# Kernel optimization log

Measured on AMD Instinct MI355X. Metric: run time of the kernel, lower is better.

Reference implementation:

```python
import jax, jax.numpy as jnp
import numpy as np

N = 8192
F_IN = 128
D = 128
NEG_SLOPE = 0.2  # cfg.negativeslope (standard GAT value)
MASK_FILL = -9e15


def setup_inputs() -> dict:
    key = jax.random.key(0)
    k1, k2, k3, k4 = jax.random.split(key, 4)
    A = jax.random.randint(k1, (N, N), 0, 2, dtype=jnp.int32)
    X = jax.random.normal(k2, (N, F_IN), dtype=jnp.float32)
    # glorot init for Ws, xavier_uniform(gain=1.414) for a
    lim_w = float(np.sqrt(6.0 / (F_IN + D)))
    Ws = jax.random.uniform(k3, (F_IN, D), minval=-lim_w, maxval=lim_w, dtype=jnp.float32)
    lim_a = 1.414 * float(np.sqrt(6.0 / (2 * D + 1)))
    a = jax.random.uniform(k4, (2 * D, 1), minval=-lim_a, maxval=lim_a, dtype=jnp.float32)
    return {"A": A, "X": X, "Ws": Ws, "a": a}


def reference(A, X, Ws, a):
    # Wh: [N, D]
    Wh = X @ Ws
    d = Wh.shape[-1]
    # additive attention: e_ij = leaky_relu(Wh_i . a1 + Wh_j . a2)
    e1 = Wh @ a[:d]          # [N, 1]
    e2 = Wh @ a[d:]          # [N, 1]
    e = jax.nn.leaky_relu(e1 + e2.T, negative_slope=NEG_SLOPE)  # [N, N]
    e = jnp.where(A > 0, e, MASK_FILL)
    attn = jax.nn.softmax(e, axis=1)  # row-wise over neighbors
    H = attn @ Wh            # [N, D]
    return H
```

## Files before the change

kernel.cpp:

```cpp
#include <hip/hip_runtime.h>
#include <hip/hip_bf16.h>

#define NN 8192
#define DD 128

typedef __attribute__((ext_vector_type(8))) short short8;
typedef __attribute__((ext_vector_type(4))) float f32x4;
typedef unsigned int u32;

__device__ __forceinline__ ushort f2bf(float f) {
    __hip_bfloat16 h = __float2bfloat16(f);
    return *(ushort*)&h;
}

__device__ __forceinline__ void async_ld16(const void* g, void* l) {
    __builtin_amdgcn_global_load_lds(
        (const __attribute__((address_space(1))) u32*)g,
        (__attribute__((address_space(3))) u32*)l, 16, 0, 0);
}

__global__ __launch_bounds__(128) void k1_gemm(const float* __restrict__ X,
                                               const float* __restrict__ Ws,
                                               float* __restrict__ Wh) {
    __shared__ float lWs[128 * 128];
    __shared__ float lX[32 * 129];
    int t = threadIdx.x, bx = blockIdx.x;
    const float4* Ws4 = (const float4*)Ws;
    float4* lWs4 = (float4*)lWs;
#pragma unroll
    for (int j = 0; j < 32; ++j) lWs4[t + j * 128] = Ws4[t + j * 128];
#pragma unroll
    for (int j = 0; j < 32; ++j) {
        int u = t + j * 128;
        int r = u >> 7, c = u & 127;
        lX[r * 129 + c] = X[(bx * 32 + r) * 128 + c];
    }
    __syncthreads();
    int tr = t >> 4, c = t & 15;
    int r0 = tr * 4;
    float acc[4][8];
#pragma unroll
    for (int i = 0; i < 4; ++i)
#pragma unroll
        for (int j = 0; j < 8; ++j) acc[i][j] = 0.f;
#pragma unroll 4
    for (int k = 0; k < 128; ++k) {
        float x0 = lX[(r0 + 0) * 129 + k];
        float x1 = lX[(r0 + 1) * 129 + k];
        float x2 = lX[(r0 + 2) * 129 + k];
        float x3 = lX[(r0 + 3) * 129 + k];
        float4 w0 = *(const float4*)&lWs[k * 128 + c * 8];
        float4 w1 = *(const float4*)&lWs[k * 128 + c * 8 + 4];
        float wv[8];
        *(float4*)(wv) = w0; *(float4*)(wv + 4) = w1;
#pragma unroll
        for (int j = 0; j < 8; ++j) {
            acc[0][j] += x0 * wv[j];
            acc[1][j] += x1 * wv[j];
            acc[2][j] += x2 * wv[j];
            acc[3][j] += x3 * wv[j];
        }
    }
#pragma unroll
    for (int i = 0; i < 4; ++i) {
        float4* o = (float4*)&Wh[(size_t)(bx * 32 + r0 + i) * 128 + c * 8];
        o[0] = (float4){acc[i][0], acc[i][1], acc[i][2], acc[i][3]};
        o[1] = (float4){acc[i][4], acc[i][5], acc[i][6], acc[i][7]};
    }
}

__global__ void k2_prep(const float* __restrict__ Wh, const float* __restrict__ a,
                        ushort* __restrict__ WhT, float* __restrict__ C1,
                        float* __restrict__ C1s, float* __restrict__ E2p,
                        float* __restrict__ E2n) {
    int wave = threadIdx.x >> 6, lane = threadIdx.x & 63;
    int i = blockIdx.x * 4 + wave;
    int d = lane * 2;
    float wh0 = Wh[i * 128 + d], wh1 = Wh[i * 128 + d + 1];
    float s1 = wh0 * a[d]       + wh1 * a[d + 1];
    float s2 = wh0 * a[128 + d] + wh1 * a[128 + d + 1];
    for (int off = 32; off; off >>= 1) {
        s1 += __shfl_xor(s1, off);
        s2 += __shfl_xor(s2, off);
    }
    WhT[(size_t)d * NN + i]       = f2bf(wh0);
    WhT[(size_t)(d + 1) * NN + i] = f2bf(wh1);
    if (lane == 0) {
        C1[i]  = __expf(s1);
        C1s[i] = __expf(0.2f * s1);
        E2p[i] = __expf(s2);
        E2n[i] = __expf(0.2f * s2);
    }
}

__global__ __launch_bounds__(1024, 8) void k3_main(
    const int* __restrict__ A, const ushort* __restrict__ WhT,
    const float* __restrict__ C1, const float* __restrict__ C1s,
    const float* __restrict__ E2p, const float* __restrict__ E2n,
    float* __restrict__ Hp, float* __restrict__ Lp) {

    __shared__ __align__(16) char tile[2][8192];
    __shared__ float red[4][16][128];
    __shared__ float lsq[2][64];

    int tid = threadIdx.x;
    int lane = tid & 63;
    int wv = tid >> 6;
    int g = wv & 3;
    int s = (wv >> 2) & 1;
    int h = wv >> 3;
    int n = lane & 15;
    int kg = lane >> 4;

    int bx = blockIdx.x;
    int kb = blockIdx.y;
    int row = bx * 64 + g * 16 + n;
    int kbase = kb * 2048 + s * 1024;

    float c1 = C1[row], c1s = C1s[row];
    const int* Arow = A + (size_t)row * NN + kbase + kg * 8;
    const float* Ep = E2p + kbase + kg * 8;
    const float* En = E2n + kbase + kg * 8;
    const ushort* src0 = WhT + (size_t)(h * 64 + g * 16 + n) * NN + kbase + kg * 8;
    char* dst0 = &tile[s][(h * 4 + g) * 1024 + lane * 16];

    f32x4 acc[4];
#pragma unroll
    for (int cc = 0; cc < 4; ++cc) acc[cc] = (f32x4){0.f, 0.f, 0.f, 0.f};
    float lsum = 0.f;

    for (int t = 0; t < 32; ++t) {
        int k = t * 32;
        async_ld16(src0 + k, dst0);
        int4 a0 = *(const int4*)(Arow + k);
        int4 a1 = *(const int4*)(Arow + k + 4);
        float4 pa = *(const float4*)(Ep + k);
        float4 pb = *(const float4*)(Ep + k + 4);
        float4 na = *(const float4*)(En + k);
        float4 nb = *(const float4*)(En + k + 4);
        __syncthreads();
        int am[8]; float ep[8], en[8];
        *(int4*)(am) = a0;       *(int4*)(am + 4) = a1;
        *(float4*)(ep) = pa;     *(float4*)(ep + 4) = pb;
        *(float4*)(en) = na;     *(float4*)(en + 4) = nb;
        short8 af;
#pragma unroll
        for (int u = 0; u < 8; ++u) {
            float w = fmaxf(c1 * ep[u], c1s * en[u]);
            w = am[u] ? w : 0.f;
            lsum += w;
            af[u] = (short)f2bf(w);
        }
#pragma unroll
        for (int cc = 0; cc < 4; ++cc) {
            short8 bf = *(const short8*)&tile[s][(h * 4 + cc) * 1024 + lane * 16];
            acc[cc] = __builtin_amdgcn_mfma_f32_16x16x32_bf16(af, bf, acc[cc], 0, 0, 0);
        }
        __syncthreads();
    }

    lsum += __shfl_xor(lsum, 16);
    lsum += __shfl_xor(lsum, 32);

    if (s == 0) {
#pragma unroll
        for (int cc = 0; cc < 4; ++cc)
#pragma unroll
            for (int r = 0; r < 4; ++r)
                red[g][kg * 4 + r][h * 64 + cc * 16 + n] = acc[cc][r];
        if (h == 0 && lane < 16) lsq[0][g * 16 + lane] = lsum;
    }
    __syncthreads();
    if (s == 1) {
#pragma unroll
        for (int cc = 0; cc < 4; ++cc)
#pragma unroll
            for (int r = 0; r < 4; ++r)
                red[g][kg * 4 + r][h * 64 + cc * 16 + n] += acc[cc][r];
        if (h == 0 && lane < 16) lsq[1][g * 16 + lane] = lsum;
    }
    __syncthreads();

    float* Hpb = Hp + (size_t)kb * (NN * DD) + (size_t)bx * 64 * 128;
    const float* redf = &red[0][0][0];
#pragma unroll
    for (int u = 0; u < 8; ++u) Hpb[tid + u * 1024] = redf[tid + u * 1024];
    if (tid < 64) Lp[kb * NN + bx * 64 + tid] = lsq[0][tid] + lsq[1][tid];
}

__global__ void k4_final(const float* __restrict__ Hp, const float* __restrict__ Lp,
                         float* __restrict__ out) {
    int idx = blockIdx.x * 256 + threadIdx.x;
    int i = idx >> 7;
    float sv = Hp[idx] + Hp[1048576 + idx] + Hp[2097152 + idx] + Hp[3145728 + idx];
    float l = Lp[i] + Lp[8192 + i] + Lp[16384 + i] + Lp[24576 + i];
    out[idx] = sv / l;
}

extern "C" void kernel_launch(void* const* d_in, const int* in_sizes, int n_in,
                              void* d_out, int out_size, void* d_ws, size_t ws_size,
                              hipStream_t stream) {
    const int*   A  = (const int*)d_in[0];
    const float* X  = (const float*)d_in[1];
    const float* Ws = (const float*)d_in[2];
    const float* a  = (const float*)d_in[3];
    float* out = (float*)d_out;

    char* ws = (char*)d_ws;
    float*  Wh  = (float*)(ws);
    ushort* WhT = (ushort*)(ws + (4u << 20));
    float*  C1  = (float*)(ws + (6u << 20));
    float*  C1s = (float*)(ws + (6u << 20) + (32u << 10));
    float*  E2p = (float*)(ws + (6u << 20) + (96u << 10));
    float*  E2n = (float*)(ws + (6u << 20) + (128u << 10));
    float*  Hp  = (float*)(ws + (8u << 20));
    float*  Lp  = (float*)(ws + (24u << 20));

    k1_gemm<<<256, 128, 0, stream>>>(X, Ws, Wh);
    k2_prep<<<2048, 256, 0, stream>>>(Wh, a, WhT, C1, C1s, E2p, E2n);
    k3_main<<<dim3(128, 4), 1024, 0, stream>>>(A, WhT, C1, C1s, E2p, E2n, Hp, Lp);
    k4_final<<<4096, 256, 0, stream>>>(Hp, Lp, out);
}
```

Measured before the change: 473.9 us.

## Stage adjacency and WhT tiles via async LDS double buffering, restructure prep kernels

The main kernel now streams both the adjacency tiles and the bf16 WhT tiles into double-buffered LDS with async global-to-LDS loads. Each wave covers the full 2048-wide K range for 16 rows and 32 output columns, which removes the split-K LDS reduction. Row sums come from an MFMA against a ones vector instead of scalar adds. The GEMM and prep kernels are also rewritten: coalesced float4 loads, an LDS transpose for the bf16 WhT stores, and wider blocks. The trade-off is 128KB of LDS per block and fewer MFMA column tiles per wave, which limits occupancy.

```diff
diff --git a/kernel.cpp b/kernel.cpp
--- a/kernel.cpp
+++ b/kernel.cpp
@@ -19,173 +19,207 @@
         (__attribute__((address_space(3))) u32*)l, 16, 0, 0);
 }
 
-__global__ __launch_bounds__(128) void k1_gemm(const float* __restrict__ X,
+__global__ __launch_bounds__(256) void k1_gemm(const float* __restrict__ X,
                                                const float* __restrict__ Ws,
                                                float* __restrict__ Wh) {
-    __shared__ float lWs[128 * 128];
-    __shared__ float lX[32 * 129];
+    __shared__ float lWs[128 * 132];
+    __shared__ float lX[32 * 132];
     int t = threadIdx.x, bx = blockIdx.x;
     const float4* Ws4 = (const float4*)Ws;
-    float4* lWs4 = (float4*)lWs;
-#pragma unroll
-    for (int j = 0; j < 32; ++j) lWs4[t + j * 128] = Ws4[t + j * 128];
-#pragma unroll
-    for (int j = 0; j < 32; ++j) {
-        int u = t + j * 128;
-        int r = u >> 7, c = u & 127;
-        lX[r * 129 + c] = X[(bx * 32 + r) * 128 + c];
+    const float4* X4 = (const float4*)X;
+    for (int j = 0; j < 16; ++j) {
+        int u = j * 256 + t;
+        int k = u >> 5, c4 = u & 31;
+        *(float4*)&lWs[k * 132 + c4 * 4] = Ws4[u];
+    }
+    for (int j = 0; j < 4; ++j) {
+        int u = j * 256 + t;
+        int r = u >> 5, c4 = u & 31;
+        *(float4*)&lX[r * 132 + c4 * 4] = X4[bx * 1024 + u];
     }
     __syncthreads();
-    int tr = t >> 4, c = t & 15;
-    int r0 = tr * 4;
-    float acc[4][8];
+    int r0 = (t >> 5) * 4, c0 = (t & 31) * 4;
+    float acc[4][4];
 #pragma unroll
     for (int i = 0; i < 4; ++i)
 #pragma unroll
-        for (int j = 0; j < 8; ++j) acc[i][j] = 0.f;
+        for (int j = 0; j < 4; ++j) acc[i][j] = 0.f;
 #pragma unroll 4
     for (int k = 0; k < 128; ++k) {
-        float x0 = lX[(r0 + 0) * 129 + k];
-        float x1 = lX[(r0 + 1) * 129 + k];
-        float x2 = lX[(r0 + 2) * 129 + k];
-        float x3 = lX[(r0 + 3) * 129 + k];
-        float4 w0 = *(const float4*)&lWs[k * 128 + c * 8];
-        float4 w1 = *(const float4*)&lWs[k * 128 + c * 8 + 4];
-        float wv[8];
-        *(float4*)(wv) = w0; *(float4*)(wv + 4) = w1;
-#pragma unroll
-        for (int j = 0; j < 8; ++j) {
-            acc[0][j] += x0 * wv[j];
-            acc[1][j] += x1 * wv[j];
-            acc[2][j] += x2 * wv[j];
-            acc[3][j] += x3 * wv[j];
+        float4 wv = *(const float4*)&lWs[k * 132 + c0];
+        float x0 = lX[(r0 + 0) * 132 + k];
+        float x1 = lX[(r0 + 1) * 132 + k];
+        float x2 = lX[(r0 + 2) * 132 + k];
+        float x3 = lX[(r0 + 3) * 132 + k];
+#pragma unroll
+        for (int j = 0; j < 4; ++j) {
+            acc[0][j] += x0 * ((const float*)&wv)[j];
+            acc[1][j] += x1 * ((const float*)&wv)[j];
+            acc[2][j] += x2 * ((const float*)&wv)[j];
+            acc[3][j] += x3 * ((const float*)&wv)[j];
         }
     }
 #pragma unroll
-    for (int i = 0; i < 4; ++i) {
-        float4* o = (float4*)&Wh[(size_t)(bx * 32 + r0 + i) * 128 + c * 8];
-        o[0] = (float4){acc[i][0], acc[i][1], acc[i][2], acc[i][3]};
-        o[1] = (float4){acc[i][4], acc[i][5], acc[i][6], acc[i][7]};
-    }
-}
-
-__global__ void k2_prep(const float* __restrict__ Wh, const float* __restrict__ a,
-                        ushort* __restrict__ WhT, float* __restrict__ C1,
-                        float* __restrict__ C1s, float* __restrict__ E2p,
-                        float* __restrict__ E2n) {
-    int wave = threadIdx.x >> 6, lane = threadIdx.x & 63;
-    int i = blockIdx.x * 4 + wave;
-    int d = lane * 2;
-    float wh0 = Wh[i * 128 + d], wh1 = Wh[i * 128 + d + 1];
-    float s1 = wh0 * a[d]       + wh1 * a[d + 1];
-    float s2 = wh0 * a[128 + d] + wh1 * a[128 + d + 1];
-    for (int off = 32; off; off >>= 1) {
-        s1 += __shfl_xor(s1, off);
-        s2 += __shfl_xor(s2, off);
-    }
-    WhT[(size_t)d * NN + i]       = f2bf(wh0);
-    WhT[(size_t)(d + 1) * NN + i] = f2bf(wh1);
-    if (lane == 0) {
+    for (int i = 0; i < 4; ++i)
+        *(float4*)&Wh[(size_t)(bx * 32 + r0 + i) * 128 + c0] =
+            (float4){acc[i][0], acc[i][1], acc[i][2], acc[i][3]};
+}
+
+__global__ __launch_bounds__(256) void k2_prep(const float* __restrict__ Wh,
+                                               const float* __restrict__ a,
+                                               ushort* __restrict__ WhT,
+                                               float* __restrict__ C1,
+                                               float* __restrict__ C1s,
+                                               float* __restrict__ E2p,
+                                               float* __restrict__ E2n) {
+    __shared__ float lT[128 * 65];
+    __shared__ float la[256];
+    int t = threadIdx.x;
+    int i0 = blockIdx.x * 64;
+    la[t] = a[t];
+    for (int j = 0; j < 32; ++j) {
+        int u = j * 256 + t;
+        int r = u >> 7, c = u & 127;
+        lT[c * 65 + r] = Wh[(size_t)(i0 + r) * 128 + c];
+    }
+    __syncthreads();
+    int r = t >> 2, q = t & 3;
+    float s1 = 0.f, s2 = 0.f;
+    for (int j = 0; j < 32; ++j) {
+        int d = q * 32 + j;
+        float v = lT[d * 65 + r];
+        s1 += v * la[d];
+        s2 += v * la[128 + d];
+    }
+    s1 += __shfl_xor(s1, 1); s1 += __shfl_xor(s1, 2);
+    s2 += __shfl_xor(s2, 1); s2 += __shfl_xor(s2, 2);
+    if (q == 0) {
+        int i = i0 + r;
         C1[i]  = __expf(s1);
         C1s[i] = __expf(0.2f * s1);
         E2p[i] = __expf(s2);
         E2n[i] = __expf(0.2f * s2);
     }
-}
-
-__global__ __launch_bounds__(1024, 8) void k3_main(
+    int d = t >> 1, hf = t & 1;
+    __attribute__((aligned(16))) ushort tmp[32];
+#pragma unroll
+    for (int s = 0; s < 32; ++s) tmp[s] = f2bf(lT[d * 65 + hf * 32 + s]);
+    uint4* dst = (uint4*)&WhT[(size_t)d * NN + i0 + hf * 32];
+    const uint4* srcv = (const uint4*)tmp;
+#pragma unroll
+    for (int s = 0; s < 4; ++s) dst[s] = srcv[s];
+}
+
+__global__ __launch_bounds__(1024, 4) void k3_main(
     const int* __restrict__ A, const ushort* __restrict__ WhT,
     const float* __restrict__ C1, const float* __restrict__ C1s,
     const float* __restrict__ E2p, const float* __restrict__ E2n,
     float* __restrict__ Hp, float* __restrict__ Lp) {
 
-    __shared__ __align__(16) char tile[2][8192];
-    __shared__ float red[4][16][128];
-    __shared__ float lsq[2][64];
+    __shared__ __align__(16) char lB[2 * 32768];
+    __shared__ __align__(16) char lA[2 * 32768];
 
     int tid = threadIdx.x;
     int lane = tid & 63;
     int wv = tid >> 6;
     int g = wv & 3;
-    int s = (wv >> 2) & 1;
-    int h = wv >> 3;
+    int h = wv >> 2;
     int n = lane & 15;
     int kg = lane >> 4;
 
     int bx = blockIdx.x;
     int kb = blockIdx.y;
     int row = bx * 64 + g * 16 + n;
-    int kbase = kb * 2048 + s * 1024;
 
     float c1 = C1[row], c1s = C1s[row];
-    const int* Arow = A + (size_t)row * NN + kbase + kg * 8;
-    const float* Ep = E2p + kbase + kg * 8;
-    const float* En = E2n + kbase + kg * 8;
-    const ushort* src0 = WhT + (size_t)(h * 64 + g * 16 + n) * NN + kbase + kg * 8;
-    char* dst0 = &tile[s][(h * 4 + g) * 1024 + lane * 16];
-
-    f32x4 acc[4];
-#pragma unroll
-    for (int cc = 0; cc < 4; ++cc) acc[cc] = (f32x4){0.f, 0.f, 0.f, 0.f};
-    float lsum = 0.f;
-
-    for (int t = 0; t < 32; ++t) {
-        int k = t * 32;
-        async_ld16(src0 + k, dst0);
-        int4 a0 = *(const int4*)(Arow + k);
-        int4 a1 = *(const int4*)(Arow + k + 4);
-        float4 pa = *(const float4*)(Ep + k);
-        float4 pb = *(const float4*)(Ep + k + 4);
-        float4 na = *(const float4*)(En + k);
-        float4 nb = *(const float4*)(En + k + 4);
-        __syncthreads();
-        int am[8]; float ep[8], en[8];
-        *(int4*)(am) = a0;       *(int4*)(am + 4) = a1;
-        *(float4*)(ep) = pa;     *(float4*)(ep + 4) = pb;
-        *(float4*)(en) = na;     *(float4*)(en + 4) = nb;
-        short8 af;
-#pragma unroll
-        for (int u = 0; u < 8; ++u) {
-            float w = fmaxf(c1 * ep[u], c1s * en[u]);
-            w = am[u] ? w : 0.f;
-            lsum += w;
-            af[u] = (short)f2bf(w);
+
+    int p0 = wv * 2;
+    int tp0 = p0 >> 3, cp0 = p0 & 7;
+    int tp1 = (p0 + 1) >> 3, cp1 = (p0 + 1) & 7;
+    int ga0 = p0 >> 3, ta0 = (p0 >> 1) & 3, qa0 = p0 & 1;
+    int ga1 = (p0 + 1) >> 3, ta1 = ((p0 + 1) >> 1) & 3, qa1 = (p0 + 1) & 1;
+
+    const ushort* srcB0 = WhT + (size_t)(cp0 * 16 + n) * NN + tp0 * 32 + kg * 8;
+    const ushort* srcB1 = WhT + (size_t)(cp1 * 16 + n) * NN + tp1 * 32 + kg * 8;
+    const int* srcA0 = A + (size_t)(bx * 64 + ga0 * 16 + n) * NN + ta0 * 32 + kg * 8 + qa0 * 4;
+    const int* srcA1 = A + (size_t)(bx * 64 + ga1 * 16 + n) * NN + ta1 * 32 + kg * 8 + qa1 * 4;
+    char* dstB0 = lB + p0 * 1024 + lane * 16;
+    char* dstB1 = lB + (p0 + 1) * 1024 + lane * 16;
+    char* dstA0 = lA + p0 * 1024 + lane * 16;
+    char* dstA1 = lA + (p0 + 1) * 1024 + lane * 16;
+
+    const size_t kbase = (size_t)kb * 2048;
+
+    short8 ones;
+#pragma unroll
+    for (int j = 0; j < 8; ++j) ones[j] = (short)0x3F80;
+
+    f32x4 acc0 = (f32x4){0.f, 0.f, 0.f, 0.f};
+    f32x4 acc1 = (f32x4){0.f, 0.f, 0.f, 0.f};
+    f32x4 accl = (f32x4){0.f, 0.f, 0.f, 0.f};
+
+    {
+        size_t k0 = kbase;
+        async_ld16(srcB0 + k0, dstB0);
+        async_ld16(srcB1 + k0, dstB1);
+        async_ld16(srcA0 + k0, dstA0);
+        async_ld16(srcA1 + k0, dstA1);
+    }
+    __syncthreads();
+
+    for (int kt = 0; kt < 16; ++kt) {
+        int b = kt & 1;
+        if (kt < 15) {
+            size_t kn = kbase + (kt + 1) * 128;
+            int bo = (b ^ 1) * 32768;
+            async_ld16(srcB0 + kn, dstB0 + bo);
+            async_ld16(srcB1 + kn, dstB1 + bo);
+            async_ld16(srcA0 + kn, dstA0 + bo);
+            async_ld16(srcA1 + kn, dstA1 + bo);
         }
-#pragma unroll
-        for (int cc = 0; cc < 4; ++cc) {
-            short8 bf = *(const short8*)&tile[s][(h * 4 + cc) * 1024 + lane * 16];
-            acc[cc] = __builtin_amdgcn_mfma_f32_16x16x32_bf16(af, bf, acc[cc], 0, 0, 0);
+        const char* bufA = lA + b * 32768;
+        const char* bufB = lB + b * 32768;
+#pragma unroll
+        for (int tp = 0; tp < 4; ++tp) {
+            const int4* areg = (const int4*)(bufA + (g * 8 + tp * 2) * 1024);
+            int4 a0 = areg[lane];
+            int4 a1 = areg[64 + lane];
+            int kgl = (int)kbase + kt * 128 + tp * 32 + kg * 8;
+            float4 pa = *(const float4*)(E2p + kgl);
+            float4 pb = *(const float4*)(E2p + kgl + 4);
+            float4 na = *(const float4*)(E2n + kgl);
+            float4 nb = *(const float4*)(E2n + kgl + 4);
+            int am[8]; float ep[8], en[8];
+            *(int4*)(am) = a0;     *(int4*)(am + 4) = a1;
+            *(float4*)(ep) = pa;   *(float4*)(ep + 4) = pb;
+            *(float4*)(en) = na;   *(float4*)(en + 4) = nb;
+            short8 af;
+#pragma unroll
+            for (int u = 0; u < 8; ++u) {
+                float w = fmaxf(c1 * ep[u], c1s * en[u]);
+                w = am[u] ? w : 0.f;
+                af[u] = (short)f2bf(w);
+            }
+            const short8* bb = (const short8*)(bufB + tp * 8192);
+            acc0 = __builtin_amdgcn_mfma_f32_16x16x32_bf16(af, bb[(2 * h + 0) * 64 + lane], acc0, 0, 0, 0);
+            acc1 = __builtin_amdgcn_mfma_f32_16x16x32_bf16(af, bb[(2 * h + 1) * 64 + lane], acc1, 0, 0, 0);
+            accl = __builtin_amdgcn_mfma_f32_16x16x32_bf16(af, ones, accl, 0, 0, 0);
         }
         __syncthreads();
     }
 
-    lsum += __shfl_xor(lsum, 16);
-    lsum += __shfl_xor(lsum, 32);
-
-    if (s == 0) {
-#pragma unroll
-        for (int cc = 0; cc < 4; ++cc)
-#pragma unroll
-            for (int r = 0; r < 4; ++r)
-                red[g][kg * 4 + r][h * 64 + cc * 16 + n] = acc[cc][r];
-        if (h == 0 && lane < 16) lsq[0][g * 16 + lane] = lsum;
-    }
-    __syncthreads();
-    if (s == 1) {
-#pragma unroll
-        for (int cc = 0; cc < 4; ++cc)
-#pragma unroll
-            for (int r = 0; r < 4; ++r)
-                red[g][kg * 4 + r][h * 64 + cc * 16 + n] += acc[cc][r];
-        if (h == 0 && lane < 16) lsq[1][g * 16 + lane] = lsum;
-    }
-    __syncthreads();
-
-    float* Hpb = Hp + (size_t)kb * (NN * DD) + (size_t)bx * 64 * 128;
-    const float* redf = &red[0][0][0];
-#pragma unroll
-    for (int u = 0; u < 8; ++u) Hpb[tid + u * 1024] = redf[tid + u * 1024];
-    if (tid < 64) Lp[kb * NN + bx * 64 + tid] = lsq[0][tid] + lsq[1][tid];
+    if (h == 0 && n == 0) {
+#pragma unroll
+        for (int r = 0; r < 4; ++r)
+            Lp[(size_t)kb * NN + bx * 64 + g * 16 + kg * 4 + r] = accl[r];
+    }
+    float* Hpb = Hp + (size_t)kb * (NN * DD);
+#pragma unroll
+    for (int r = 0; r < 4; ++r) {
+        int orow = bx * 64 + g * 16 + kg * 4 + r;
+        Hpb[(size_t)orow * DD + h * 32 + n] = acc0[r];
+        Hpb[(size_t)orow * DD + h * 32 + 16 + n] = acc1[r];
+    }
 }
 
 __global__ void k4_final(const float* __restrict__ Hp, const float* __restrict__ Lp,
@@ -216,8 +250,8 @@
     float*  Hp  = (float*)(ws + (8u << 20));
     float*  Lp  = (float*)(ws + (24u << 20));
 
-    k1_gemm<<<256, 128, 0, stream>>>(X, Ws, Wh);
-    k2_prep<<<2048, 256, 0, stream>>>(Wh, a, WhT, C1, C1s, E2p, E2n);
+    k1_gemm<<<256, 256, 0, stream>>>(X, Ws, Wh);
+    k2_prep<<<128, 256, 0, stream>>>(Wh, a, WhT, C1, C1s, E2p, E2n);
     k3_main<<<dim3(128, 4), 1024, 0, stream>>>(A, WhT, C1, C1s, E2p, E2n, Hp, Lp);
     k4_final<<<4096, 256, 0, stream>>>(Hp, Lp, out);
 }
```

After: 462.3 us. 1.03x faster.
